# Optimization experiments

Hardware: AMD Instinct MI355X
Metric: run time of the kernel (lower is better)

Reference implementation:

```python
import jax, jax.numpy as jnp
import numpy as np

HEADS = 8

def setup_inputs() -> dict:
    key = jax.random.key(0)
    ks = jax.random.split(key, 7)
    B, N, M, C = 4, 2048, 2048, 512
    s = 0.02
    return {
        "hidden_states": jax.random.normal(ks[0], (B, N, C), jnp.float32),
        "encoder_states": jax.random.normal(ks[1], (B, M, C), jnp.float32),
        "Wq": jax.random.normal(ks[2], (C, C), jnp.float32) * s,
        "Wk": jax.random.normal(ks[3], (C, C), jnp.float32) * s,
        "Wv": jax.random.normal(ks[4], (C, C), jnp.float32) * s,
        "Wo": jax.random.normal(ks[5], (C, C), jnp.float32) * s,
        "bo": jnp.zeros((C,), jnp.float32),
    }

def reference(hidden_states, encoder_states, Wq, Wk, Wv, Wo, bo):
    B, N, C = hidden_states.shape
    M = encoder_states.shape[1]
    H = HEADS
    dh = C // H
    scale = dh ** -0.5  # q.shape[-1] ** -0.5 in FlashAttentionFunction / attn.scale
    # projections (to_q/to_k/to_v, no bias as in diffusers CrossAttention)
    q = (hidden_states @ Wq).reshape(B, N, H, dh).transpose(0, 2, 1, 3)   # [B,H,N,dh]
    k = (encoder_states @ Wk).reshape(B, M, H, dh).transpose(0, 2, 1, 3)  # [B,H,M,dh]
    v = (encoder_states @ Wv).reshape(B, M, H, dh).transpose(0, 2, 1, 3)  # [B,H,M,dh]
    # baddbmm(scores) -> softmax -> bmm(values); no mask, non-causal
    scores = jnp.einsum('bhnd,bhmd->bhnm', q, k) * scale                  # [B,H,N,M]
    probs = jax.nn.softmax(scores, axis=-1)
    out = jnp.einsum('bhnm,bhmd->bhnd', probs, v)                         # [B,H,N,dh]
    out = out.transpose(0, 2, 1, 3).reshape(B, N, C)                      # batch_to_head_dim
    return out @ Wo + bo                                                  # to_out[0]; to_out[1] is dropout (identity at eval)
```

## Files before the change

kernel.cpp:

```cpp
#include <hip/hip_runtime.h>
#include <stdint.h>
#include <stddef.h>

typedef __bf16 bf16x8 __attribute__((ext_vector_type(8)));
typedef float f32x4 __attribute__((ext_vector_type(4)));
typedef float f32x16 __attribute__((ext_vector_type(16)));
typedef int int4v __attribute__((ext_vector_type(4)));
typedef unsigned short u16;
typedef unsigned int u32;

__device__ __forceinline__ u16 f2bf(float f) {
    union { float f; unsigned u; } x; x.f = f;
    unsigned r = x.u + 0x7fffu + ((x.u >> 16) & 1u);
    return (u16)(r >> 16);
}

__device__ __forceinline__ float fexp2(float x) { return __builtin_amdgcn_exp2f(x); }

__device__ __forceinline__ u32 cvtpk(float lo, float hi) {
    u32 r;
    asm("v_cvt_pk_bf16_f32 %0, %1, %2" : "=v"(r) : "v"(lo), "v"(hi));
    return r;
}

__device__ __forceinline__ void perm32swap(u32& a, u32& b) {
    asm("v_permlane32_swap_b32 %0, %1" : "+v"(a), "+v"(b));
}

__device__ __forceinline__ f32x16 mfma32(bf16x8 a, bf16x8 b, f32x16 c) {
    return __builtin_amdgcn_mfma_f32_32x32x16_bf16(a, b, c, 0, 0, 0);
}

__device__ __forceinline__ void gl16(const void* g, void* l) {
    __builtin_amdgcn_global_load_lds(
        (const __attribute__((address_space(1))) void*)g,
        (__attribute__((address_space(3))) void*)l, 16, 0, 0);
}

__global__ __launch_bounds__(256) void wtrans4(
        const float* __restrict__ Wq, const float* __restrict__ Wk,
        const float* __restrict__ Wv, const float* __restrict__ Wo,
        u16* __restrict__ oq, u16* __restrict__ ok,
        u16* __restrict__ ov, u16* __restrict__ oo) {
    const int z = blockIdx.z;
    const float* W = (z == 0) ? Wq : (z == 1) ? Wk : (z == 2) ? Wv : Wo;
    u16* O = (z == 0) ? oq : (z == 1) ? ok : (z == 2) ? ov : oo;
    int t  = blockIdx.x * 256 + threadIdx.x;
    int g  = t >> 12;
    int k0 = (t >> 9) & 7;
    int n  = t & 511;
    float v[8];
#pragma unroll
    for (int j = 0; j < 8; ++j)
        v[j] = W[(size_t)(k0 * 64 + g * 8 + j) * 512 + n];
    int gs = g ^ (n & 7);
    u16* dst = O + ((size_t)(k0 * 512 + n) * 8 + gs) * 8;
    ushort4 a, b;
    a.x = f2bf(v[0]); a.y = f2bf(v[1]); a.z = f2bf(v[2]); a.w = f2bf(v[3]);
    b.x = f2bf(v[4]); b.y = f2bf(v[5]); b.z = f2bf(v[6]); b.w = f2bf(v[7]);
    *(ushort4*)dst = a;
    *(ushort4*)(dst + 4) = b;
}

__global__ __launch_bounds__(256) void gemm_qkv(
        const float* __restrict__ hidden, const float* __restrict__ enc,
        const u16* __restrict__ wq, const u16* __restrict__ wk, const u16* __restrict__ wv,
        u16* __restrict__ qo, u16* __restrict__ ko, u16* __restrict__ vo) {
    __shared__ __align__(16) u16 As[128 * 64];
    __shared__ __align__(16) u16 Bs[128 * 64];
    const int z = blockIdx.z;
    const float* A = (z == 0) ? hidden : enc;
    const u16* Bp = (z == 0) ? wq : (z == 1) ? wk : wv;
    const int tid = threadIdx.x, lane = tid & 63, wave = tid >> 6;
    const int wr = (wave >> 1) * 64, wc = (wave & 1) * 64;
    const int brow = blockIdx.x * 128, bcol = blockIdx.y * 128;
    const int lrow = lane & 15;
    const int sr = tid >> 3, sc = tid & 7;

    f32x4 acc[4][4] = {};

    for (int k0s = 0; k0s < 8; ++k0s) {
        const u16* bsrc = Bp + ((size_t)(k0s * 512 + bcol) * 64) + (size_t)(wave * 256 + lane) * 8;
#pragma unroll
        for (int i = 0; i < 4; ++i)
            gl16(bsrc + i * 512, (char*)Bs + wave * 4096 + i * 1024);
#pragma unroll
        for (int i = 0; i < 4; ++i) {
            int r = i * 32 + sr;
            const float* src = A + (size_t)(brow + r) * 512 + k0s * 64 + sc * 8;
            float4 f0 = *(const float4*)src, f1 = *(const float4*)(src + 4);
            int4v w;
            w[0] = cvtpk(f0.x, f0.y); w[1] = cvtpk(f0.z, f0.w);
            w[2] = cvtpk(f1.x, f1.y); w[3] = cvtpk(f1.z, f1.w);
            *(int4v*)((char*)As + r * 128 + ((sc ^ (r & 7)) << 4)) = w;
        }
        __syncthreads();
#pragma unroll
        for (int kc = 0; kc < 2; ++kc) {
            const int kg = kc * 4 + (lane >> 4);
            bf16x8 af[4], bfr[4];
#pragma unroll
            for (int m = 0; m < 4; ++m) {
                int r = wr + m * 16 + lrow;
                af[m] = *(const bf16x8*)((char*)As + r * 128 + ((kg ^ (r & 7)) << 4));
            }
#pragma unroll
            for (int n = 0; n < 4; ++n) {
                int r = wc + n * 16 + lrow;
                bfr[n] = *(const bf16x8*)((char*)Bs + r * 128 + ((kg ^ (r & 7)) << 4));
            }
#pragma unroll
            for (int m = 0; m < 4; ++m)
#pragma unroll
                for (int n = 0; n < 4; ++n)
                    acc[m][n] = __builtin_amdgcn_mfma_f32_16x16x32_bf16(af[m], bfr[n], acc[m][n], 0, 0, 0);
        }
        __syncthreads();
    }

#pragma unroll
    for (int m = 0; m < 4; ++m) {
        int gr0 = brow + wr + m * 16 + ((lane >> 4) << 2);
#pragma unroll
        for (int n = 0; n < 4; ++n) {
            int gc = bcol + wc + n * 16 + lrow;
            int hh = gc >> 6, d = gc & 63;
            if (z == 2) {
                int b = gr0 >> 11, mm = gr0 & 2047;
                ushort4 pk;
                pk.x = f2bf(acc[m][n][0]); pk.y = f2bf(acc[m][n][1]);
                pk.z = f2bf(acc[m][n][2]); pk.w = f2bf(acc[m][n][3]);
                *(ushort4*)(vo + ((size_t)(b * 8 + hh) * 64 + d) * 2048 + mm) = pk;
            } else {
                u16* dst = (z == 0) ? qo : ko;
                const float s = (z == 0) ? 0.125f * 1.44269504f : 1.0f;
#pragma unroll
                for (int j = 0; j < 4; ++j) {
                    int gr = gr0 + j;
                    int b = gr >> 11, nn = gr & 2047;
                    dst[((size_t)(b * 8 + hh) * 2048 + nn) * 64 + d] = f2bf(acc[m][n][j] * s);
                }
            }
        }
    }
}

__global__ __launch_bounds__(256) void gemm_out(
        const u16* __restrict__ A, const u16* __restrict__ Bp,
        const float* __restrict__ bias, float* __restrict__ out) {
    __shared__ __align__(16) u16 As[128 * 64];
    __shared__ __align__(16) u16 Bs[64 * 64];
    const int tid = threadIdx.x, lane = tid & 63, wave = tid >> 6;
    const int wr = (wave >> 1) * 64, wc = (wave & 1) * 32;
    const int brow = blockIdx.x * 128, bcol = blockIdx.y * 64;
    const int lrow = lane & 15;
    const int ar = wave * 32 + (lane >> 3), ag = lane & 7;

    f32x4 acc[4][2] = {};

    for (int k0s = 0; k0s < 8; ++k0s) {
        const u16* asrc = A + (size_t)(brow + ar) * 512 + k0s * 64 + ag * 8;
#pragma unroll
        for (int i = 0; i < 4; ++i)
            gl16(asrc + (size_t)(i * 8) * 512, (char*)As + wave * 4096 + i * 1024);
        const u16* bsrc = Bp + ((size_t)(k0s * 512 + bcol) * 64) + (size_t)(wave * 128 + lane) * 8;
#pragma unroll
        for (int i = 0; i < 2; ++i)
            gl16(bsrc + i * 512, (char*)Bs + wave * 2048 + i * 1024);
        __syncthreads();
#pragma unroll
        for (int kc = 0; kc < 2; ++kc) {
            const int kg = kc * 4 + (lane >> 4);
            bf16x8 af[4], bfr[2];
#pragma unroll
            for (int m = 0; m < 4; ++m) {
                int r = wr + m * 16 + lrow;
                af[m] = *(const bf16x8*)((char*)As + r * 128 + ((kg ^ (r & 7)) << 4));
            }
#pragma unroll
            for (int n = 0; n < 2; ++n) {
                int r = wc + n * 16 + lrow;
                bfr[n] = *(const bf16x8*)((char*)Bs + r * 128 + ((kg ^ (r & 7)) << 4));
            }
#pragma unroll
            for (int m = 0; m < 4; ++m)
#pragma unroll
                for (int n = 0; n < 2; ++n)
                    acc[m][n] = __builtin_amdgcn_mfma_f32_16x16x32_bf16(af[m], bfr[n], acc[m][n], 0, 0, 0);
        }
        __syncthreads();
    }

#pragma unroll
    for (int m = 0; m < 4; ++m) {
        int gr0 = brow + wr + m * 16 + ((lane >> 4) << 2);
#pragma unroll
        for (int n = 0; n < 2; ++n) {
            int gc = bcol + wc + n * 16 + lrow;
            float bv = bias[gc];
#pragma unroll
            for (int j = 0; j < 4; ++j)
                out[(size_t)(gr0 + j) * 512 + gc] = acc[m][n][j] + bv;
        }
    }
}

__global__ __launch_bounds__(256, 2) void flash_attn(
        const u16* __restrict__ Q, const u16* __restrict__ K,
        const u16* __restrict__ VT, u16* __restrict__ Oa) {
    __shared__ __align__(16) char smem[65536];

    const int tid  = threadIdx.x;
    const int lane = tid & 63;
    const int wave = tid >> 6;
    const int qg   = wave >> 1;
    const int half = wave & 1;
    const int ql   = lane & 31;
    const int hl   = lane >> 5;
    const int bid  = blockIdx.x;
    const int lid  = (bid & 7) * 64 + (bid >> 3);
    const int bh   = lid >> 4;
    const int qt   = lid & 15;
    const int qbase = qt * 128 + qg * 64;

    bf16x8 qf[2][4];
#pragma unroll
    for (int sq = 0; sq < 2; ++sq)
#pragma unroll
        for (int kc = 0; kc < 4; ++kc)
            qf[sq][kc] = *(const bf16x8*)(Q + ((size_t)bh * 2048 + qbase + sq * 32 + ql) * 64 + kc * 16 + hl * 8);

    const int srow = lane >> 3;
    const int sgr  = (lane & 7) ^ srow;
    const u16* ksrc = K  + (size_t)bh * 131072 + (size_t)(half * 1024 + srow) * 64 + sgr * 8;
    const u16* vsrc = VT + (size_t)bh * 131072 + (size_t)srow * 2048 + half * 1024 + sgr * 8;
    char* kdst = smem + half * 8192;
    char* vdst = smem + 16384 + half * 8192;

#define STAGE(b_, t_) do { \
    if (qg == 0) { \
        const u16* s_ = ksrc + (size_t)(t_) * 4096; \
        char* d_ = kdst + (b_) * 32768; \
        _Pragma("unroll") \
        for (int i = 0; i < 8; ++i) gl16(s_ + i * 512, d_ + i * 1024); \
    } else { \
        const u16* s_ = vsrc + (t_) * 64; \
        char* d_ = vdst + (b_) * 32768; \
        _Pragma("unroll") \
        for (int i = 0; i < 8; ++i) gl16(s_ + (size_t)i * 16384, d_ + i * 1024); \
    } \
} while (0)

    f32x16 acc00 = {}, acc01 = {}, acc10 = {}, acc11 = {};
    float ls[2][4] = {};

    STAGE(0, 0);
    __syncthreads();

    for (int t = 0; t < 16; ++t) {
        const int b = t & 1;
        if (t < 15) STAGE(b ^ 1, t + 1);
        const char* Kt = smem + b * 32768 + half * 8192;
        const char* Vt = smem + b * 32768 + 16384 + half * 8192;

#pragma unroll
        for (int ks = 0; ks < 2; ++ks) {
            bf16x8 kf[4];
#pragma unroll
            for (int kc = 0; kc < 4; ++kc) {
                int kr = ks * 32 + ql;
                kf[kc] = *(const bf16x8*)(Kt + kr * 128 + (((kc * 2 + hl) ^ (kr & 7)) << 4));
            }
            bf16x8 vf[2][2];
#pragma unroll
            for (int jl = 0; jl < 2; ++jl)
#pragma unroll
                for (int dh2 = 0; dh2 < 2; ++dh2) {
                    int dr = dh2 * 32 + ql;
                    vf[jl][dh2] = *(const bf16x8*)(Vt + dr * 128 + (((ks * 4 + jl * 2 + hl) ^ (dr & 7)) << 4));
                }

            f32x16 st0 = {}, st1 = {};
            __builtin_amdgcn_s_setprio(1);
#pragma unroll
            for (int kc = 0; kc < 4; ++kc) {
                st0 = mfma32(kf[kc], qf[0][kc], st0);
                st1 = mfma32(kf[kc], qf[1][kc], st1);
            }
            __builtin_amdgcn_s_setprio(0);

#pragma unroll
            for (int r = 0; r < 16; r += 4) {
                st0[r]   = fexp2(st0[r]);   ls[0][0] += st0[r];
                st0[r+1] = fexp2(st0[r+1]); ls[0][1] += st0[r+1];
                st0[r+2] = fexp2(st0[r+2]); ls[0][2] += st0[r+2];
                st0[r+3] = fexp2(st0[r+3]); ls[0][3] += st0[r+3];
                st1[r]   = fexp2(st1[r]);   ls[1][0] += st1[r];
                st1[r+1] = fexp2(st1[r+1]); ls[1][1] += st1[r+1];
                st1[r+2] = fexp2(st1[r+2]); ls[1][2] += st1[r+2];
                st1[r+3] = fexp2(st1[r+3]); ls[1][3] += st1[r+3];
            }

            __builtin_amdgcn_s_setprio(1);
#pragma unroll
            for (int jl = 0; jl < 2; ++jl) {
                u32 A0 = cvtpk(st0[8*jl+0], st0[8*jl+1]);
                u32 A1 = cvtpk(st0[8*jl+2], st0[8*jl+3]);
                u32 B0 = cvtpk(st0[8*jl+4], st0[8*jl+5]);
                u32 B1 = cvtpk(st0[8*jl+6], st0[8*jl+7]);
                perm32swap(A0, B0);
                perm32swap(A1, B1);
                union { bf16x8 v; u32 u[4]; } bb0;
                bb0.u[0] = A0; bb0.u[1] = A1; bb0.u[2] = B0; bb0.u[3] = B1;
                acc00 = mfma32(vf[jl][0], bb0.v, acc00);
                acc01 = mfma32(vf[jl][1], bb0.v, acc01);
                u32 C0 = cvtpk(st1[8*jl+0], st1[8*jl+1]);
                u32 C1 = cvtpk(st1[8*jl+2], st1[8*jl+3]);
                u32 D0 = cvtpk(st1[8*jl+4], st1[8*jl+5]);
                u32 D1 = cvtpk(st1[8*jl+6], st1[8*jl+7]);
                perm32swap(C0, D0);
                perm32swap(C1, D1);
                union { bf16x8 v; u32 u[4]; } bb1;
                bb1.u[0] = C0; bb1.u[1] = C1; bb1.u[2] = D0; bb1.u[3] = D1;
                acc10 = mfma32(vf[jl][0], bb1.v, acc10);
                acc11 = mfma32(vf[jl][1], bb1.v, acc11);
            }
            __builtin_amdgcn_s_setprio(0);
        }
        __syncthreads();
    }
#undef STAGE

    float lsum0 = (ls[0][0] + ls[0][1]) + (ls[0][2] + ls[0][3]);
    float lsum1 = (ls[1][0] + ls[1][1]) + (ls[1][2] + ls[1][3]);
    lsum0 += __shfl_xor(lsum0, 32);
    lsum1 += __shfl_xor(lsum1, 32);

    float* CB = (float*)smem;
    float* LS = (float*)(smem + 32768);

#define PUBQ(sq, A0, A1, LSV) do { \
    int qq = (sq) * 32 + ql; \
    float* R = CB + qg * 4096 + qq * 64; \
    _Pragma("unroll") \
    for (int rg = 0; rg < 4; ++rg) { \
        int g0 = (2 * rg + hl) ^ (qq & 15); \
        *(f32x4*)(R + g0 * 4) = f32x4{A0[4*rg], A0[4*rg+1], A0[4*rg+2], A0[4*rg+3]}; \
        int g1 = (8 + 2 * rg + hl) ^ (qq & 15); \
        *(f32x4*)(R + g1 * 4) = f32x4{A1[4*rg], A1[4*rg+1], A1[4*rg+2], A1[4*rg+3]}; \
    } \
    if (hl == 0) LS[qg * 64 + qq] = LSV; \
} while (0)

#define REDQ(sq, A0, A1, LSV) do { \
    int qq = (sq) * 32 + ql; \
    const float* R = CB + qg * 4096 + qq * 64; \
    _Pragma("unroll") \
    for (int rg = 0; rg < 4; ++rg) { \
        int g0 = (2 * rg + hl) ^ (qq & 15); \
        f32x4 v0 = *(const f32x4*)(R + g0 * 4); \
        A0[4*rg] += v0[0]; A0[4*rg+1] += v0[1]; A0[4*rg+2] += v0[2]; A0[4*rg+3] += v0[3]; \
        int g1 = (8 + 2 * rg + hl) ^ (qq & 15); \
        f32x4 v1 = *(const f32x4*)(R + g1 * 4); \
        A1[4*rg] += v1[0]; A1[4*rg+1] += v1[1]; A1[4*rg+2] += v1[2]; A1[4*rg+3] += v1[3]; \
    } \
    LSV += LS[qg * 64 + qq]; \
} while (0)

    if (half == 1) {
        PUBQ(0, acc00, acc01, lsum0);
        PUBQ(1, acc10, acc11, lsum1);
    }
    __syncthreads();
    if (half == 0) {
        REDQ(0, acc00, acc01, lsum0);
        REDQ(1, acc10, acc11, lsum1);
        float inv0 = 1.0f / lsum0, inv1 = 1.0f / lsum1;
        int b_ = bh >> 3, hd = bh & 7;
#define STOQ(sq, A0, A1, INV) do { \
        int qrow = qbase + (sq) * 32 + ql; \
        u16* orow = Oa + ((size_t)b_ * 2048 + qrow) * 512 + hd * 64; \
        _Pragma("unroll") \
        for (int rg = 0; rg < 4; ++rg) { \
            int d00 = ((rg ^ (qrow & 7)) << 3) + hl * 4; \
            ushort4 p0; \
            p0.x = f2bf(A0[4*rg] * INV);   p0.y = f2bf(A0[4*rg+1] * INV); \
            p0.z = f2bf(A0[4*rg+2] * INV); p0.w = f2bf(A0[4*rg+3] * INV); \
            *(ushort4*)(orow + d00) = p0; \
            int d01 = (((4 + rg) ^ (qrow & 7)) << 3) + hl * 4; \
            ushort4 p1; \
            p1.x = f2bf(A1[4*rg] * INV);   p1.y = f2bf(A1[4*rg+1] * INV); \
            p1.z = f2bf(A1[4*rg+2] * INV); p1.w = f2bf(A1[4*rg+3] * INV); \
            *(ushort4*)(orow + d01) = p1; \
        } \
} while (0)
        STOQ(0, acc00, acc01, inv0);
        STOQ(1, acc10, acc11, inv1);
#undef STOQ
    }
#undef PUBQ
#undef REDQ
}

extern "C" void kernel_launch(void* const* d_in, const int* in_sizes, int n_in,
                              void* d_out, int out_size, void* d_ws, size_t ws_size,
                              hipStream_t stream) {
    const float* hidden = (const float*)d_in[0];
    const float* enc    = (const float*)d_in[1];
    const float* Wq     = (const float*)d_in[2];
    const float* Wk     = (const float*)d_in[3];
    const float* Wv     = (const float*)d_in[4];
    const float* Wo     = (const float*)d_in[5];
    const float* bo     = (const float*)d_in[6];
    float* out = (float*)d_out;

    char* ws = (char*)d_ws;
    const size_t MB = 1ull << 20;
    u16* q_bf  = (u16*)(ws + 0 * MB);
    u16* k_bf  = (u16*)(ws + 8 * MB);
    u16* vt_bf = (u16*)(ws + 16 * MB);
    u16* at_bf = (u16*)(ws + 24 * MB);
    u16* wq_t  = (u16*)(ws + 32 * MB);
    u16* wk_t  = (u16*)(ws + 32 * MB + 512 * 1024);
    u16* wv_t  = (u16*)(ws + 33 * MB);
    u16* wo_t  = (u16*)(ws + 33 * MB + 512 * 1024);

    dim3 wg(128, 1, 4);
    wtrans4<<<wg, 256, 0, stream>>>(Wq, Wk, Wv, Wo, wq_t, wk_t, wv_t, wo_t);

    dim3 qkvg(64, 4, 3);
    gemm_qkv<<<qkvg, 256, 0, stream>>>(hidden, enc, wq_t, wk_t, wv_t, q_bf, k_bf, vt_bf);

    flash_attn<<<512, 256, 0, stream>>>(q_bf, k_bf, vt_bf, at_bf);

    dim3 og(64, 8);
    gemm_out<<<og, 256, 0, stream>>>(at_bf, wo_t, bo, out);
}
```

Measured before the change: 87.72 us.

## Split attention KV range four ways per block with per-wave private buffers

Each block now handles 64 queries, and each of its four waves processes a quarter of the key/value sequence. Every wave stages its own K/V tiles into a private LDS double buffer, so the main loop needs only vmcnt waits and no block-wide barriers. The grid doubles to 1024 blocks, and the partial outputs and row sums are combined through LDS in a three-step serial reduction at the end. In exchange, Q fragments are loaded by every wave for every query, each global load is smaller, and the final reduction costs extra barriers and LDS traffic.

Result: slower. 116.1 us (+32.3%).

```diff
diff --git a/kernel.cpp b/kernel.cpp
--- a/kernel.cpp
+++ b/kernel.cpp
@@ -212,16 +212,14 @@
 
     const int tid  = threadIdx.x;
     const int lane = tid & 63;
-    const int wave = tid >> 6;
-    const int qg   = wave >> 1;
-    const int half = wave & 1;
+    const int qtr  = tid >> 6;
     const int ql   = lane & 31;
     const int hl   = lane >> 5;
     const int bid  = blockIdx.x;
-    const int lid  = (bid & 7) * 64 + (bid >> 3);
-    const int bh   = lid >> 4;
-    const int qt   = lid & 15;
-    const int qbase = qt * 128 + qg * 64;
+    const int lid  = (bid & 7) * 128 + (bid >> 3);
+    const int bh   = lid >> 5;
+    const int qt   = lid & 31;
+    const int qbase = qt * 64;
 
     bf16x8 qf[2][4];
 #pragma unroll
@@ -230,104 +228,97 @@
         for (int kc = 0; kc < 4; ++kc)
             qf[sq][kc] = *(const bf16x8*)(Q + ((size_t)bh * 2048 + qbase + sq * 32 + ql) * 64 + kc * 16 + hl * 8);
 
-    const int srow = lane >> 3;
-    const int sgr  = (lane & 7) ^ srow;
-    const u16* ksrc = K  + (size_t)bh * 131072 + (size_t)(half * 1024 + srow) * 64 + sgr * 8;
-    const u16* vsrc = VT + (size_t)bh * 131072 + (size_t)srow * 2048 + half * 1024 + sgr * 8;
-    char* kdst = smem + half * 8192;
-    char* vdst = smem + 16384 + half * 8192;
+    const u16* Kb = K  + (size_t)bh * 131072 + ((size_t)qtr * 512 + ql) * 64 + hl * 8;
+    const u16* Vb = VT + (size_t)bh * 131072 + (size_t)ql * 2048 + qtr * 512 + hl * 8;
+    char* mybuf = smem + qtr * 16384;
 
 #define STAGE(b_, t_) do { \
-    if (qg == 0) { \
-        const u16* s_ = ksrc + (size_t)(t_) * 4096; \
-        char* d_ = kdst + (b_) * 32768; \
-        _Pragma("unroll") \
-        for (int i = 0; i < 8; ++i) gl16(s_ + i * 512, d_ + i * 1024); \
-    } else { \
-        const u16* s_ = vsrc + (t_) * 64; \
-        char* d_ = vdst + (b_) * 32768; \
-        _Pragma("unroll") \
-        for (int i = 0; i < 8; ++i) gl16(s_ + (size_t)i * 16384, d_ + i * 1024); \
-    } \
+    const u16* ks_ = Kb + (size_t)(t_) * 2048; \
+    char* kd_ = mybuf + (b_) * 8192; \
+    gl16(ks_,      kd_); \
+    gl16(ks_ + 16, kd_ + 1024); \
+    gl16(ks_ + 32, kd_ + 2048); \
+    gl16(ks_ + 48, kd_ + 3072); \
+    const u16* vs_ = Vb + (t_) * 32; \
+    char* vd_ = kd_ + 4096; \
+    gl16(vs_,              vd_);           \
+    gl16(vs_ + 65536,      vd_ + 1024);    \
+    gl16(vs_ + 16,         vd_ + 2048);    \
+    gl16(vs_ + 16 + 65536, vd_ + 3072);    \
 } while (0)
 
     f32x16 acc00 = {}, acc01 = {}, acc10 = {}, acc11 = {};
     float ls[2][4] = {};
 
     STAGE(0, 0);
-    __syncthreads();
-
+    int buf = 0;
     for (int t = 0; t < 16; ++t) {
-        const int b = t & 1;
-        if (t < 15) STAGE(b ^ 1, t + 1);
-        const char* Kt = smem + b * 32768 + half * 8192;
-        const char* Vt = smem + b * 32768 + 16384 + half * 8192;
-
-#pragma unroll
-        for (int ks = 0; ks < 2; ++ks) {
-            bf16x8 kf[4];
-#pragma unroll
-            for (int kc = 0; kc < 4; ++kc) {
-                int kr = ks * 32 + ql;
-                kf[kc] = *(const bf16x8*)(Kt + kr * 128 + (((kc * 2 + hl) ^ (kr & 7)) << 4));
-            }
-            bf16x8 vf[2][2];
-#pragma unroll
-            for (int jl = 0; jl < 2; ++jl)
-#pragma unroll
-                for (int dh2 = 0; dh2 < 2; ++dh2) {
-                    int dr = dh2 * 32 + ql;
-                    vf[jl][dh2] = *(const bf16x8*)(Vt + dr * 128 + (((ks * 4 + jl * 2 + hl) ^ (dr & 7)) << 4));
-                }
-
-            f32x16 st0 = {}, st1 = {};
-            __builtin_amdgcn_s_setprio(1);
-#pragma unroll
-            for (int kc = 0; kc < 4; ++kc) {
-                st0 = mfma32(kf[kc], qf[0][kc], st0);
-                st1 = mfma32(kf[kc], qf[1][kc], st1);
-            }
-            __builtin_amdgcn_s_setprio(0);
-
-#pragma unroll
-            for (int r = 0; r < 16; r += 4) {
-                st0[r]   = fexp2(st0[r]);   ls[0][0] += st0[r];
-                st0[r+1] = fexp2(st0[r+1]); ls[0][1] += st0[r+1];
-                st0[r+2] = fexp2(st0[r+2]); ls[0][2] += st0[r+2];
-                st0[r+3] = fexp2(st0[r+3]); ls[0][3] += st0[r+3];
-                st1[r]   = fexp2(st1[r]);   ls[1][0] += st1[r];
-                st1[r+1] = fexp2(st1[r+1]); ls[1][1] += st1[r+1];
-                st1[r+2] = fexp2(st1[r+2]); ls[1][2] += st1[r+2];
-                st1[r+3] = fexp2(st1[r+3]); ls[1][3] += st1[r+3];
-            }
-
-            __builtin_amdgcn_s_setprio(1);
-#pragma unroll
-            for (int jl = 0; jl < 2; ++jl) {
-                u32 A0 = cvtpk(st0[8*jl+0], st0[8*jl+1]);
-                u32 A1 = cvtpk(st0[8*jl+2], st0[8*jl+3]);
-                u32 B0 = cvtpk(st0[8*jl+4], st0[8*jl+5]);
-                u32 B1 = cvtpk(st0[8*jl+6], st0[8*jl+7]);
-                perm32swap(A0, B0);
-                perm32swap(A1, B1);
-                union { bf16x8 v; u32 u[4]; } bb0;
-                bb0.u[0] = A0; bb0.u[1] = A1; bb0.u[2] = B0; bb0.u[3] = B1;
-                acc00 = mfma32(vf[jl][0], bb0.v, acc00);
-                acc01 = mfma32(vf[jl][1], bb0.v, acc01);
-                u32 C0 = cvtpk(st1[8*jl+0], st1[8*jl+1]);
-                u32 C1 = cvtpk(st1[8*jl+2], st1[8*jl+3]);
-                u32 D0 = cvtpk(st1[8*jl+4], st1[8*jl+5]);
-                u32 D1 = cvtpk(st1[8*jl+6], st1[8*jl+7]);
-                perm32swap(C0, D0);
-                perm32swap(C1, D1);
-                union { bf16x8 v; u32 u[4]; } bb1;
-                bb1.u[0] = C0; bb1.u[1] = C1; bb1.u[2] = D0; bb1.u[3] = D1;
-                acc10 = mfma32(vf[jl][0], bb1.v, acc10);
-                acc11 = mfma32(vf[jl][1], bb1.v, acc11);
-            }
-            __builtin_amdgcn_s_setprio(0);
-        }
-        __syncthreads();
+        if (t < 15) {
+            STAGE(buf ^ 1, t + 1);
+            asm volatile("s_waitcnt vmcnt(8)" ::: "memory");
+        } else {
+            asm volatile("s_waitcnt vmcnt(0)" ::: "memory");
+        }
+        __builtin_amdgcn_sched_barrier(0);
+
+        const u16* Kt = (const u16*)(mybuf + buf * 8192);
+        const u16* Vt = Kt + 2048;
+        bf16x8 kf[4], vf[4];
+#pragma unroll
+        for (int kc = 0; kc < 4; ++kc)
+            kf[kc] = *(const bf16x8*)(Kt + kc * 512 + lane * 8);
+#pragma unroll
+        for (int s = 0; s < 4; ++s)
+            vf[s] = *(const bf16x8*)(Vt + s * 512 + lane * 8);
+
+        f32x16 st0 = {}, st1 = {};
+        __builtin_amdgcn_s_setprio(1);
+#pragma unroll
+        for (int kc = 0; kc < 4; ++kc) {
+            st0 = mfma32(kf[kc], qf[0][kc], st0);
+            st1 = mfma32(kf[kc], qf[1][kc], st1);
+        }
+        __builtin_amdgcn_s_setprio(0);
+
+#pragma unroll
+        for (int r = 0; r < 16; r += 4) {
+            st0[r]   = fexp2(st0[r]);   ls[0][0] += st0[r];
+            st0[r+1] = fexp2(st0[r+1]); ls[0][1] += st0[r+1];
+            st0[r+2] = fexp2(st0[r+2]); ls[0][2] += st0[r+2];
+            st0[r+3] = fexp2(st0[r+3]); ls[0][3] += st0[r+3];
+            st1[r]   = fexp2(st1[r]);   ls[1][0] += st1[r];
+            st1[r+1] = fexp2(st1[r+1]); ls[1][1] += st1[r+1];
+            st1[r+2] = fexp2(st1[r+2]); ls[1][2] += st1[r+2];
+            st1[r+3] = fexp2(st1[r+3]); ls[1][3] += st1[r+3];
+        }
+
+        __builtin_amdgcn_s_setprio(1);
+#pragma unroll
+        for (int jl = 0; jl < 2; ++jl) {
+            u32 A0 = cvtpk(st0[8*jl+0], st0[8*jl+1]);
+            u32 A1 = cvtpk(st0[8*jl+2], st0[8*jl+3]);
+            u32 B0 = cvtpk(st0[8*jl+4], st0[8*jl+5]);
+            u32 B1 = cvtpk(st0[8*jl+6], st0[8*jl+7]);
+            perm32swap(A0, B0);
+            perm32swap(A1, B1);
+            union { bf16x8 v; u32 u[4]; } bb0;
+            bb0.u[0] = A0; bb0.u[1] = A1; bb0.u[2] = B0; bb0.u[3] = B1;
+            acc00 = mfma32(vf[jl*2+0], bb0.v, acc00);
+            acc01 = mfma32(vf[jl*2+1], bb0.v, acc01);
+            u32 C0 = cvtpk(st1[8*jl+0], st1[8*jl+1]);
+            u32 C1 = cvtpk(st1[8*jl+2], st1[8*jl+3]);
+            u32 D0 = cvtpk(st1[8*jl+4], st1[8*jl+5]);
+            u32 D1 = cvtpk(st1[8*jl+6], st1[8*jl+7]);
+            perm32swap(C0, D0);
+            perm32swap(C1, D1);
+            union { bf16x8 v; u32 u[4]; } bb1;
+            bb1.u[0] = C0; bb1.u[1] = C1; bb1.u[2] = D0; bb1.u[3] = D1;
+            acc10 = mfma32(vf[jl*2+0], bb1.v, acc10);
+            acc11 = mfma32(vf[jl*2+1], bb1.v, acc11);
+        }
+        __builtin_amdgcn_s_setprio(0);
+
+        buf ^= 1;
     }
 #undef STAGE
 
@@ -337,11 +328,11 @@
     lsum1 += __shfl_xor(lsum1, 32);
 
     float* CB = (float*)smem;
-    float* LS = (float*)(smem + 32768);
+    float* LS = (float*)(smem + 16384);
 
 #define PUBQ(sq, A0, A1, LSV) do { \
     int qq = (sq) * 32 + ql; \
-    float* R = CB + qg * 4096 + qq * 64; \
+    float* R = CB + qq * 64; \
     _Pragma("unroll") \
     for (int rg = 0; rg < 4; ++rg) { \
         int g0 = (2 * rg + hl) ^ (qq & 15); \
@@ -349,12 +340,12 @@
         int g1 = (8 + 2 * rg + hl) ^ (qq & 15); \
         *(f32x4*)(R + g1 * 4) = f32x4{A1[4*rg], A1[4*rg+1], A1[4*rg+2], A1[4*rg+3]}; \
     } \
-    if (hl == 0) LS[qg * 64 + qq] = LSV; \
+    if (hl == 0) LS[qq] = LSV; \
 } while (0)
 
 #define REDQ(sq, A0, A1, LSV) do { \
     int qq = (sq) * 32 + ql; \
-    const float* R = CB + qg * 4096 + qq * 64; \
+    const float* R = CB + qq * 64; \
     _Pragma("unroll") \
     for (int rg = 0; rg < 4; ++rg) { \
         int g0 = (2 * rg + hl) ^ (qq & 15); \
@@ -364,17 +355,24 @@
         f32x4 v1 = *(const f32x4*)(R + g1 * 4); \
         A1[4*rg] += v1[0]; A1[4*rg+1] += v1[1]; A1[4*rg+2] += v1[2]; A1[4*rg+3] += v1[3]; \
     } \
-    LSV += LS[qg * 64 + qq]; \
+    LSV += LS[qq]; \
 } while (0)
 
-    if (half == 1) {
-        PUBQ(0, acc00, acc01, lsum0);
-        PUBQ(1, acc10, acc11, lsum1);
-    }
     __syncthreads();
-    if (half == 0) {
-        REDQ(0, acc00, acc01, lsum0);
-        REDQ(1, acc10, acc11, lsum1);
+    for (int p = 1; p < 4; ++p) {
+        if (qtr == p) {
+            PUBQ(0, acc00, acc01, lsum0);
+            PUBQ(1, acc10, acc11, lsum1);
+        }
+        __syncthreads();
+        if (qtr == 0) {
+            REDQ(0, acc00, acc01, lsum0);
+            REDQ(1, acc10, acc11, lsum1);
+        }
+        __syncthreads();
+    }
+
+    if (qtr == 0) {
         float inv0 = 1.0f / lsum0, inv1 = 1.0f / lsum1;
         int b_ = bh >> 3, hd = bh & 7;
 #define STOQ(sq, A0, A1, INV) do { \
@@ -431,7 +429,7 @@
     dim3 qkvg(64, 4, 3);
     gemm_qkv<<<qkvg, 256, 0, stream>>>(hidden, enc, wq_t, wk_t, wv_t, q_bf, k_bf, vt_bf);
 
-    flash_attn<<<512, 256, 0, stream>>>(q_bf, k_bf, vt_bf, at_bf);
+    flash_attn<<<1024, 256, 0, stream>>>(q_bf, k_bf, vt_bf, at_bf);
 
     dim3 og(64, 8);
     gemm_out<<<og, 256, 0, stream>>>(at_bf, wo_t, bo, out);
```
